# Kernel tuning notes

Hardware: AMD Instinct MI355X
Metric: run time of the kernel (lower is better)

## Reference

```python
import jax, jax.numpy as jnp
import numpy as np

B, S, HID = 1, 2048, 2048
NH, NKV, HD = 32, 8, 64
INTER = 8192
EPS = 1e-6


def rmsnorm(x, w, eps=EPS):
    xf = x.astype(jnp.float32)
    inv = jax.lax.rsqrt(jnp.mean(xf * xf, axis=-1, keepdims=True) + eps)
    return (xf * inv * w).astype(x.dtype)


def rope(x, sin_t, cos_t):
    # x: [B, S, H, D]; sin/cos: [S, D//2]
    sin = sin_t[None, :, None, :]
    cos = cos_t[None, :, None, :]
    d2 = x.shape[-1] // 2
    x0, x1 = x[..., :d2], x[..., d2:]
    return jnp.concatenate((x0 * cos - x1 * sin, x0 * sin + x1 * cos), axis=-1)


def setup_inputs() -> dict:
    key = jax.random.key(0)
    ks = jax.random.split(key, 12)
    hidden_states = jax.random.normal(ks[0], (B, S, HID), dtype=jnp.float32)
    # realistic RoPE tables
    inv_freq = 1.0 / (10000.0 ** (np.arange(0, HD // 2, dtype=np.float32) * 2.0 / HD))
    ang = np.arange(S, dtype=np.float32)[:, None] * inv_freq[None, :]
    sin_table = jnp.asarray(np.sin(ang))
    cos_table = jnp.asarray(np.cos(ang))
    s = 0.02
    return {
        "hidden_states": hidden_states,
        "sin_table": sin_table,
        "cos_table": cos_table,
        "ln1_w": jnp.ones((HID,), jnp.float32),
        "ln2_w": jnp.ones((HID,), jnp.float32),
        "wq": jax.random.normal(ks[1], (HID, NH * HD), jnp.float32) * s,
        "wk": jax.random.normal(ks[2], (HID, NKV * HD), jnp.float32) * s,
        "wv": jax.random.normal(ks[3], (HID, NKV * HD), jnp.float32) * s,
        "wo": jax.random.normal(ks[4], (NH * HD, HID), jnp.float32) * s,
        "w_gate": jax.random.normal(ks[5], (HID, INTER), jnp.float32) * s,
        "w_up": jax.random.normal(ks[6], (HID, INTER), jnp.float32) * s,
        "w_down": jax.random.normal(ks[7], (INTER, HID), jnp.float32) * s,
    }


def attention(x, sin_t, cos_t, wq, wk, wv, wo):
    b, s, _ = x.shape
    q = (x @ wq).reshape(b, s, NH, HD)
    k = (x @ wk).reshape(b, s, NKV, HD)
    v = (x @ wv).reshape(b, s, NKV, HD).transpose(0, 2, 1, 3)  # [B,Hk,S,D]
    q = rope(q, sin_t, cos_t).transpose(0, 2, 1, 3)  # [B,Hq,S,D]
    k = rope(k, sin_t, cos_t).transpose(0, 2, 1, 3)  # [B,Hk,S,D]
    g = NH // NKV
    k = jnp.repeat(k, g, axis=1)
    v = jnp.repeat(v, g, axis=1)
    scale = 1.0 / np.sqrt(HD)
    scores = jnp.einsum("bhqd,bhkd->bhqk", q, k) * scale
    mask = jnp.tril(jnp.ones((s, s), dtype=bool))
    scores = jnp.where(mask, scores, -jnp.inf)
    probs = jax.nn.softmax(scores, axis=-1)
    out = jnp.einsum("bhqk,bhkd->bhqd", probs, v)
    out = out.transpose(0, 2, 1, 3).reshape(b, s, NH * HD)
    return out @ wo


def reference(hidden_states, sin_table, cos_table, ln1_w, ln2_w, wq, wk, wv, wo, w_gate, w_up, w_down):
    x = hidden_states
    x = x + attention(rmsnorm(x, ln1_w), sin_table, cos_table, wq, wk, wv, wo)
    h = rmsnorm(x, ln2_w)
    x = x + (jax.nn.silu(h @ w_gate) * (h @ w_up)) @ w_down
    return x
```

## Files before the change

kernel.cpp:

```cpp
#include <hip/hip_runtime.h>
#include <hip/hip_bf16.h>

typedef float f32x4 __attribute__((ext_vector_type(4)));
typedef unsigned int u32x4 __attribute__((ext_vector_type(4)));
typedef unsigned int u32x2 __attribute__((ext_vector_type(2)));
typedef _Float16 f16x4 __attribute__((ext_vector_type(4)));
typedef unsigned short u16;

#define S_LEN 2048
#define HID 2048
#define NHEAD 32
#define NKVH 8
#define HDIM 64

__device__ __forceinline__ unsigned short f2bf_bits(float f) {
    unsigned int u = __builtin_bit_cast(unsigned int, f);
    unsigned int r = u + 0x7fffu + ((u >> 16) & 1u);
    return (unsigned short)(r >> 16);
}
__device__ __forceinline__ float bf2f(unsigned short b) {
    unsigned int u = ((unsigned int)b) << 16;
    return __builtin_bit_cast(float, u);
}
__device__ __forceinline__ unsigned cvt_pk_bf16(float lo, float hi) {
    unsigned d;
    asm("v_cvt_pk_bf16_f32 %0, %1, %2" : "=v"(d) : "v"(lo), "v"(hi));
    return d;
}

__device__ __forceinline__ f32x4 mfma_bf16(u32x4 a, u32x4 b, f32x4 c) {
    asm("v_mfma_f32_16x16x32_bf16 %0, %1, %2, %0" : "+v"(c) : "v"(a), "v"(b));
    return c;
}

__device__ __forceinline__ void gload_lds16(const void* g, void* l) {
    __builtin_amdgcn_global_load_lds(
        (const __attribute__((address_space(1))) void*)g,
        (__attribute__((address_space(3))) void*)l, 16, 0, 0);
}

__global__ __launch_bounds__(256)
void rmsnorm_k(const float* __restrict__ x, const float* __restrict__ wgt,
               unsigned short* __restrict__ out)
{
    int row = blockIdx.x;
    int t = threadIdx.x;
    const float* xr = x + (size_t)row * HID;
    f32x4 a = *(const f32x4*)(xr + t * 8);
    f32x4 b = *(const f32x4*)(xr + t * 8 + 4);
    float s = 0.f;
#pragma unroll
    for (int i = 0; i < 4; ++i) s += a[i] * a[i] + b[i] * b[i];
#pragma unroll
    for (int off = 32; off > 0; off >>= 1) s += __shfl_down(s, off);
    __shared__ float red[4];
    if ((t & 63) == 0) red[t >> 6] = s;
    __syncthreads();
    float tot = red[0] + red[1] + red[2] + red[3];
    float inv = rsqrtf(tot * (1.0f / (float)HID) + 1e-6f);
    f32x4 wa = *(const f32x4*)(wgt + t * 8);
    f32x4 wb = *(const f32x4*)(wgt + t * 8 + 4);
    unsigned int pk[4];
#pragma unroll
    for (int i = 0; i < 2; ++i) {
        pk[i]     = (unsigned)f2bf_bits(a[2*i] * inv * wa[2*i]) |
                    ((unsigned)f2bf_bits(a[2*i+1] * inv * wa[2*i+1]) << 16);
        pk[i + 2] = (unsigned)f2bf_bits(b[2*i] * inv * wb[2*i]) |
                    ((unsigned)f2bf_bits(b[2*i+1] * inv * wb[2*i+1]) << 16);
    }
    u32x4 ov; ov[0] = pk[0]; ov[1] = pk[1]; ov[2] = pk[2]; ov[3] = pk[3];
    *(u32x4*)(out + (size_t)row * HID + t * 8) = ov;
}

__global__ __launch_bounds__(256)
void transpose_cvt(const float* __restrict__ in, unsigned short* __restrict__ out,
                   int K, int N)
{
    __shared__ unsigned short tile[64 * 65];
    int kb = blockIdx.y * 64, nb = blockIdx.x * 64;
    int t = threadIdx.x;
    int r = t >> 2, c0 = (t & 3) * 16;
    const float* src = in + (size_t)(kb + r) * N + nb + c0;
#pragma unroll
    for (int j = 0; j < 4; ++j) {
        f32x4 v = *(const f32x4*)(src + j * 4);
#pragma unroll
        for (int i = 0; i < 4; ++i)
            tile[r * 65 + c0 + j * 4 + i] = f2bf_bits(v[i]);
    }
    __syncthreads();
    unsigned short e[16];
#pragma unroll
    for (int j = 0; j < 16; ++j) e[j] = tile[(c0 + j) * 65 + r];
    u32x4 o0, o1;
#pragma unroll
    for (int j = 0; j < 4; ++j) {
        o0[j] = (unsigned)e[2*j] | ((unsigned)e[2*j+1] << 16);
        o1[j] = (unsigned)e[8 + 2*j] | ((unsigned)e[8 + 2*j+1] << 16);
    }
    unsigned short* dst = out + (size_t)(nb + r) * K + kb + c0;
    *(u32x4*)(dst) = o0;
    *(u32x4*)(dst + 8) = o1;
}

__global__ __launch_bounds__(256)
void rope_k(unsigned short* __restrict__ qkv, const float* __restrict__ sin_t,
            const float* __restrict__ cos_t)
{
    int s = blockIdx.x;
    for (int it = threadIdx.x; it < (NHEAD + NKVH) * 32; it += 256) {
        int slot = it >> 5;
        int d = it & 31;
        int col = (slot < NHEAD) ? slot * 64 + d : HID + (slot - NHEAD) * 64 + d;
        unsigned short* p = qkv + (size_t)s * 3072 + col;
        float x0 = bf2f(p[0]);
        float x1 = bf2f(p[32]);
        float c = cos_t[s * 32 + d];
        float sn = sin_t[s * 32 + d];
        p[0]  = f2bf_bits(x0 * c - x1 * sn);
        p[32] = f2bf_bits(x0 * sn + x1 * c);
    }
}

__global__ __launch_bounds__(256)
void transpose_v(const unsigned short* __restrict__ qkv, unsigned short* __restrict__ vT)
{
    __shared__ unsigned short tile[64][80];
    int kb = blockIdx.x * 64, kvh = blockIdx.y;
    int t = threadIdx.x;
    int r = t >> 2, c0 = (t & 3) * 16;
    const unsigned short* src = qkv + (size_t)(kb + r) * 3072 + 2560 + kvh * 64 + c0;
    u32x4 v0 = *(const u32x4*)(src);
    u32x4 v1 = *(const u32x4*)(src + 8);
    *(u32x4*)&tile[r][c0] = v0;
    *(u32x4*)&tile[r][c0 + 8] = v1;
    __syncthreads();
    int d = t >> 2, k0 = (t & 3) * 16;
    unsigned short e[16];
#pragma unroll
    for (int j = 0; j < 16; ++j) e[j] = tile[k0 + j][d];
    u32x4 o0, o1;
#pragma unroll
    for (int j = 0; j < 4; ++j) {
        o0[j] = (unsigned)e[2*j] | ((unsigned)e[2*j+1] << 16);
        o1[j] = (unsigned)e[8 + 2*j] | ((unsigned)e[8 + 2*j+1] << 16);
    }
    int s0 = ((k0 >> 3) ^ (d & 7)) & 7;
    int s1 = (((k0 >> 3) + 1) ^ (d & 7)) & 7;
    unsigned short* dst = vT + ((size_t)kvh * 64 + d) * 2048 + kb;
    *(u32x4*)(dst + s0 * 8) = o0;
    *(u32x4*)(dst + s1 * 8) = o1;
}

template <int EPI>
__global__ __launch_bounds__(256)
void gemm_bt(const unsigned short* __restrict__ A,
             const unsigned short* __restrict__ Bt,
             void* __restrict__ outp, const void* __restrict__ auxp,
             int M, int N, int Kc, int lda)
{
    __shared__ unsigned short As[2][128 * 32];
    __shared__ unsigned short Bs[2][128 * 32];
    int t = threadIdx.x, w = t >> 6, l = t & 63;
    int rb = blockIdx.y, cb = blockIdx.x, zb = blockIdx.z;
    int wr = w >> 1, wc = w & 1;
    int l4 = l >> 4, l15 = l & 15;
    int arow = l >> 2, acol = (l & 3) * 8;
    f32x4 acc[4][4] = {};
    const unsigned short* Ag = A + (size_t)rb * 128 * lda + (size_t)zb * Kc
                                 + (size_t)(w * 16 + arow) * lda + acol;
    const unsigned short* Bg = Bt + (size_t)cb * 128 * lda + (size_t)zb * Kc
                                 + (size_t)(w * 16 + arow) * lda + acol;
    int nk = Kc >> 5;

#define STAGE(buf, kt)                                                          \
    {                                                                           \
        const unsigned short* Agk = Ag + (size_t)(kt) * 32;                     \
        const unsigned short* Bgk = Bg + (size_t)(kt) * 32;                     \
        gload_lds16(Agk, &As[buf][w * 512]);                                    \
        gload_lds16(Agk + (size_t)64 * lda, &As[buf][(4 + w) * 512]);           \
        gload_lds16(Bgk, &Bs[buf][w * 512]);                                    \
        gload_lds16(Bgk + (size_t)64 * lda, &Bs[buf][(4 + w) * 512]);           \
    }

    STAGE(0, 0);
    __syncthreads();
    int cur = 0;
    for (int kt = 0; kt < nk; ++kt) {
        if (kt + 1 < nk) STAGE(cur ^ 1, kt + 1);
        u32x4 af[4], bfr[4];
#pragma unroll
        for (int i = 0; i < 4; ++i)
            af[i] = *(const u32x4*)(&As[cur][(wr * 64 + i * 16 + l15) * 32 + l4 * 8]);
#pragma unroll
        for (int n = 0; n < 4; ++n)
            bfr[n] = *(const u32x4*)(&Bs[cur][(wc * 64 + n * 16 + l15) * 32 + l4 * 8]);
#pragma unroll
        for (int i = 0; i < 4; ++i)
#pragma unroll
            for (int n = 0; n < 4; ++n)
                acc[i][n] = mfma_bf16(af[i], bfr[n], acc[i][n]);
        __syncthreads();
        cur ^= 1;
    }
#undef STAGE

    int row0 = rb * 128 + wr * 64 + l4 * 4;
    int col0 = cb * 128 + wc * 64 + l15;
#pragma unroll
    for (int i = 0; i < 4; ++i) {
#pragma unroll
        for (int n = 0; n < 4; ++n) {
#pragma unroll
            for (int r = 0; r < 4; ++r) {
                int row = row0 + i * 16 + r;
                int col = col0 + n * 16;
                size_t idx = (size_t)row * N + col;
                float v = acc[i][n][r];
                if (EPI == 0) {
                    ((unsigned short*)outp)[idx] = f2bf_bits(v);
                } else if (EPI == 3) {
                    ((float*)outp)[idx] = v + ((const float*)auxp)[idx];
                } else {
                    ((_Float16*)outp)[(size_t)zb * M * N + idx] = (_Float16)v;
                }
            }
        }
    }
}

template <int KK, int QUAD, int WAITN>
__device__ __forceinline__ void phase8(u16* lds, int cur, f32x4 (&acc)[8][4],
                                       u32x4 (&bfv)[4],
                                       int aoff, int boff,
                                       const u16* Asrc, const u16* Bsrc,
                                       int lda, int kt_next, bool dostage,
                                       int dst0, int dst1)
{
    const u16* ah = lds + (cur * 4 + KK * 2) * 8192 + aoff + QUAD * 2048;
    u32x4 af[4];
#pragma unroll
    for (int mi = 0; mi < 4; ++mi) af[mi] = *(const u32x4*)(ah + mi * 512);
    if (QUAD == 0) {
        const u16* bh = lds + (cur * 4 + KK * 2 + 1) * 8192 + boff;
#pragma unroll
        for (int ni = 0; ni < 4; ++ni) bfv[ni] = *(const u32x4*)(bh + ni * 512);
    }
    if (dostage) {
        const u16* src = (QUAD ? Bsrc : Asrc) + (size_t)kt_next * 64 + KK * 32;
        u16* d = lds + ((cur ^ 1) * 4 + (KK * 2 + QUAD)) * 8192;
        gload_lds16(src, d + dst0);
        gload_lds16(src + (size_t)128 * lda, d + dst1);
    }
    __builtin_amdgcn_s_barrier();
    asm volatile("s_waitcnt lgkmcnt(0)" ::: "memory");
    __builtin_amdgcn_sched_barrier(0);
    __builtin_amdgcn_s_setprio(1);
#pragma unroll
    for (int mi = 0; mi < 4; ++mi)
#pragma unroll
        for (int ni = 0; ni < 4; ++ni)
            acc[QUAD * 4 + mi][ni] = mfma_bf16(af[mi], bfv[ni], acc[QUAD * 4 + mi][ni]);
    __builtin_amdgcn_s_setprio(0);
    if (WAITN == 4) asm volatile("s_waitcnt vmcnt(4)" ::: "memory");
    else if (WAITN == 0) asm volatile("s_waitcnt vmcnt(0)" ::: "memory");
    __builtin_amdgcn_s_barrier();
}

template <int EPI>
__global__ __launch_bounds__(512, 2)
void gemm8p(const u16* __restrict__ A, const u16* __restrict__ Bt,
            void* __restrict__ outp, const void* __restrict__ auxp,
            int M, int N, int Kc, int lda)
{
    extern __shared__ u16 lds[];
    const int tid = threadIdx.x;
    const int w = tid >> 6, l = tid & 63;
    const int wm = w >> 2, wn = w & 3;
    const int l4 = l >> 4, l15 = l & 15;
    const int zb = blockIdx.y;

    int wg = blockIdx.x, nwg = gridDim.x;
    int swzb = ((nwg & 7) == 0) ? ((wg & 7) * (nwg >> 3) + (wg >> 3)) : wg;
    int rbs = M >> 8;
    int rb = swzb % rbs, cb = swzb / rbs;

    const int sw = ((tid & 3) ^ ((tid >> 3) & 3)) * 8;
    const int srow = tid >> 2;
    const u16* Asrc = A + (size_t)(rb * 256 + srow) * lda + (size_t)zb * Kc + sw;
    const u16* Bsrc = Bt + (size_t)(cb * 256 + srow) * lda + (size_t)zb * Kc + sw;
    const int dst0 = tid * 8, dst1 = (512 + tid) * 8;

    const int rswz = (l15 >> 1) & 3;
    const int aoff = (wm * 128 + l15) * 32 + (l4 ^ rswz) * 8;
    const int boff = (wn * 64 + l15) * 32 + (l4 ^ rswz) * 8;

    f32x4 acc[8][4] = {};
    u32x4 bfv[4];
    const int NT = Kc >> 6;

#pragma unroll
    for (int h = 0; h < 2; ++h) {
        const u16* sA = Asrc + h * 32;
        const u16* sB = Bsrc + h * 32;
        gload_lds16(sA, lds + (h * 2) * 8192 + dst0);
        gload_lds16(sA + (size_t)128 * lda, lds + (h * 2) * 8192 + dst1);
        gload_lds16(sB, lds + (h * 2 + 1) * 8192 + dst0);
        gload_lds16(sB + (size_t)128 * lda, lds + (h * 2 + 1) * 8192 + dst1);
    }
    asm volatile("s_waitcnt vmcnt(4)" ::: "memory");
    __builtin_amdgcn_s_barrier();

    for (int t = 0; t < NT - 1; ++t) {
        int cur = t & 1;
        phase8<0, 0, -1>(lds, cur, acc, bfv, aoff, boff, Asrc, Bsrc, lda, t + 1, true, dst0, dst1);
        phase8<0, 1,  4>(lds, cur, acc, bfv, aoff, boff, Asrc, Bsrc, lda, t + 1, true, dst0, dst1);
        phase8<1, 0, -1>(lds, cur, acc, bfv, aoff, boff, Asrc, Bsrc, lda, t + 1, true, dst0, dst1);
        phase8<1, 1,  4>(lds, cur, acc, bfv, aoff, boff, Asrc, Bsrc, lda, t + 1, true, dst0, dst1);
    }
    {
        int cur = (NT - 1) & 1;
        phase8<0, 0, -1>(lds, cur, acc, bfv, aoff, boff, Asrc, Bsrc, lda, 0, false, dst0, dst1);
        phase8<0, 1,  0>(lds, cur, acc, bfv, aoff, boff, Asrc, Bsrc, lda, 0, false, dst0, dst1);
        phase8<1, 0, -1>(lds, cur, acc, bfv, aoff, boff, Asrc, Bsrc, lda, 0, false, dst0, dst1);
        phase8<1, 1, -1>(lds, cur, acc, bfv, aoff, boff, Asrc, Bsrc, lda, 0, false, dst0, dst1);
    }

    int row0 = rb * 256 + wm * 128 + l4 * 4;
    int col0 = cb * 256 + wn * 64 + l15;
#pragma unroll
    for (int mi = 0; mi < 8; ++mi) {
#pragma unroll
        for (int ni = 0; ni < 4; ++ni) {
#pragma unroll
            for (int r = 0; r < 4; ++r) {
                int row = row0 + mi * 16 + r;
                int col = col0 + ni * 16;
                size_t idx = (size_t)row * N + col;
                float v = acc[mi][ni][r];
                if (EPI == 1) {
                    float sv = v / (1.0f + __expf(-v));
                    ((unsigned short*)outp)[idx] = f2bf_bits(sv);
                } else if (EPI == 2) {
                    float gv = bf2f(((const unsigned short*)auxp)[idx]);
                    ((unsigned short*)outp)[idx] = f2bf_bits(v * gv);
                } else {
                    ((_Float16*)outp)[(size_t)zb * M * N + idx] = (_Float16)v;
                }
            }
        }
    }
}

__global__ __launch_bounds__(256)
void reduce_add4(float* __restrict__ out, const _Float16* __restrict__ p, int n)
{
    int i = (blockIdx.x * 256 + threadIdx.x) * 4;
    f32x4 a = *(const f32x4*)(out + i);
#pragma unroll
    for (int z = 0; z < 4; ++z) {
        f16x4 h = *(const f16x4*)(p + (size_t)z * n + i);
#pragma unroll
        for (int j = 0; j < 4; ++j) a[j] += (float)h[j];
    }
    *(f32x4*)(out + i) = a;
}

__global__ __launch_bounds__(256)
void reduce_res2(float* __restrict__ out, const float* __restrict__ x,
                 const _Float16* __restrict__ p, int n)
{
    int i = (blockIdx.x * 256 + threadIdx.x) * 4;
    f32x4 a = *(const f32x4*)(x + i);
#pragma unroll
    for (int z = 0; z < 2; ++z) {
        f16x4 h = *(const f16x4*)(p + (size_t)z * n + i);
#pragma unroll
        for (int j = 0; j < 4; ++j) a[j] += (float)h[j];
    }
    *(f32x4*)(out + i) = a;
}

__global__ __launch_bounds__(256)
void attn_fwd(const unsigned short* __restrict__ qkv,
              const unsigned short* __restrict__ vT,
              unsigned short* __restrict__ out)
{
    int p = blockIdx.x, h = blockIdx.y, kvh = h >> 2;
    int t = threadIdx.x, w = t >> 6, l = t & 63;
    int l4 = l >> 4, l15 = l & 15;
    __shared__ unsigned short Ks[2][64 * 64];
    __shared__ unsigned short Vs[2][64 * 64];

    const unsigned short* Kg = qkv + HID + kvh * 64;
    const unsigned short* Vg = vT + (size_t)kvh * 64 * 2048;

    int ch0 = w * 2, ch1 = w * 2 + 1;
    int rsub = l >> 3;
    int ksw = ((l & 7) ^ (rsub & 7)) * 8;
    int vcol = (l & 7) * 8;
    int sw0 = (l4 ^ (l15 & 7)) * 8;
    int sw1 = ((l4 | 4) ^ (l15 & 7)) * 8;
    int srcA = ((l >> 4) & 1) * 32 + l15;
    int srcB = srcA + 16;
    bool hi32 = (l & 32) != 0;

#define STAGE_KV(buf, kt)                                                         \
    {                                                                             \
        gload_lds16(Kg + (size_t)((kt) * 64 + ch0 * 8 + rsub) * 3072 + ksw,       \
                    &Ks[buf][ch0 * 512]);                                         \
        gload_lds16(Kg + (size_t)((kt) * 64 + ch1 * 8 + rsub) * 3072 + ksw,       \
                    &Ks[buf][ch1 * 512]);                                         \
        gload_lds16(Vg + (size_t)(ch0 * 8 + rsub) * 2048 + (kt) * 64 + vcol,      \
                    &Vs[buf][ch0 * 512]);                                         \
        gload_lds16(Vg + (size_t)(ch1 * 8 + rsub) * 2048 + (kt) * 64 + vcol,      \
                    &Vs[buf][ch1 * 512]);                                         \
    }

    const float SC2 = 0.18033688f;
    const float THR = 44.36f;
    const float BIG = -3.0e38f;

    for (int half = 0; half < 2; ++half) {
        int qb = half ? (31 - p) : p;
        int qrow0 = qb * 64 + w * 16;
        STAGE_KV(0, 0);
        const unsigned short* qg = qkv + (size_t)(qrow0 + l15) * 3072 + h * 64 + l4 * 8;
        u32x4 aq0 = *(const u32x4*)(qg);
        u32x4 aq1 = *(const u32x4*)(qg + 32);
        f32x4 o[4] = {};
        float m = BIG, ls = 0.f;
        __syncthreads();
        int cur = 0;
        for (int kt = 0; kt <= qb; ++kt) {
            if (kt < qb) STAGE_KV(cur ^ 1, kt + 1);
            f32x4 sc[4];
#pragma unroll
            for (int n = 0; n < 4; ++n) {
                const unsigned short* kb_ = &Ks[cur][(n * 16 + l15) * 64];
                u32x4 b0 = *(const u32x4*)(kb_ + sw0);
                u32x4 b1 = *(const u32x4*)(kb_ + sw1);
                f32x4 z = {};
                z = mfma_bf16(b0, aq0, z);
                z = mfma_bf16(b1, aq1, z);
                sc[n] = z;
            }
            if (kt == qb) {
                int qloc = w * 16 + l15;
#pragma unroll
                for (int n = 0; n < 4; ++n)
#pragma unroll
                    for (int r = 0; r < 4; ++r)
                        if (n * 16 + l4 * 4 + r > qloc) sc[n][r] = BIG;
            }
            float rmax = BIG;
#pragma unroll
            for (int n = 0; n < 4; ++n)
#pragma unroll
                for (int r = 0; r < 4; ++r) rmax = fmaxf(rmax, sc[n][r]);
            rmax = fmaxf(rmax, __shfl_xor(rmax, 16));
            rmax = fmaxf(rmax, __shfl_xor(rmax, 32));
            if (__ballot(rmax - m > THR)) {
                float mn = fmaxf(m, rmax);
                float al = __builtin_exp2f((m - mn) * SC2);
                m = mn;
                ls *= al;
#pragma unroll
                for (int nd = 0; nd < 4; ++nd)
#pragma unroll
                    for (int r = 0; r < 4; ++r) o[nd][r] *= al;
            }
            float ms = m * SC2, rs = 0.f;
#pragma unroll
            for (int n = 0; n < 4; ++n)
#pragma unroll
                for (int r = 0; r < 4; ++r) {
                    float pe = __builtin_exp2f(__builtin_fmaf(sc[n][r], SC2, -ms));
                    sc[n][r] = pe;
                    rs += pe;
                }
            rs += __shfl_xor(rs, 16);
            rs += __shfl_xor(rs, 32);
            ls += rs;
            unsigned pk0[2], pk1[2], pk2[2], pk3[2];
#pragma unroll
            for (int rr = 0; rr < 2; ++rr) {
                pk0[rr] = cvt_pk_bf16(sc[0][2*rr], sc[0][2*rr+1]);
                pk1[rr] = cvt_pk_bf16(sc[1][2*rr], sc[1][2*rr+1]);
                pk2[rr] = cvt_pk_bf16(sc[2][2*rr], sc[2][2*rr+1]);
                pk3[rr] = cvt_pk_bf16(sc[3][2*rr], sc[3][2*rr+1]);
            }
            u32x4 W1, W2;
            {
                unsigned a0, a1;
                a0 = __shfl(pk0[0], srcA); a1 = __shfl(pk1[0], srcA); W1[0] = hi32 ? a1 : a0;
                a0 = __shfl(pk0[1], srcA); a1 = __shfl(pk1[1], srcA); W1[1] = hi32 ? a1 : a0;
                a0 = __shfl(pk0[0], srcB); a1 = __shfl(pk1[0], srcB); W1[2] = hi32 ? a1 : a0;
                a0 = __shfl(pk0[1], srcB); a1 = __shfl(pk1[1], srcB); W1[3] = hi32 ? a1 : a0;
                a0 = __shfl(pk2[0], srcA); a1 = __shfl(pk3[0], srcA); W2[0] = hi32 ? a1 : a0;
                a0 = __shfl(pk2[1], srcA); a1 = __shfl(pk3[1], srcA); W2[1] = hi32 ? a1 : a0;
                a0 = __shfl(pk2[0], srcB); a1 = __shfl(pk3[0], srcB); W2[2] = hi32 ? a1 : a0;
                a0 = __shfl(pk2[1], srcB); a1 = __shfl(pk3[1], srcB); W2[3] = hi32 ? a1 : a0;
            }
#pragma unroll
            for (int nd = 0; nd < 4; ++nd) {
                const unsigned short* vb = &Vs[cur][(nd * 16 + l15) * 64];
                u32x4 bv0 = *(const u32x4*)(vb + sw0);
                u32x4 bv1 = *(const u32x4*)(vb + sw1);
                o[nd] = mfma_bf16(bv0, W1, o[nd]);
                o[nd] = mfma_bf16(bv1, W2, o[nd]);
            }
            __syncthreads();
            cur ^= 1;
        }
#undef STAGE_KV
        float linv = 1.0f / ls;
        unsigned short* orow = out + (size_t)(qrow0 + l15) * HID + h * 64 + l4 * 4;
#pragma unroll
        for (int nd = 0; nd < 4; ++nd) {
            u32x2 wv;
            wv[0] = cvt_pk_bf16(o[nd][0] * linv, o[nd][1] * linv);
            wv[1] = cvt_pk_bf16(o[nd][2] * linv, o[nd][3] * linv);
            *(u32x2*)(orow + nd * 16) = wv;
        }
    }
}

extern "C" void kernel_launch(void* const* d_in, const int* in_sizes, int n_in,
                              void* d_out, int out_size, void* d_ws, size_t ws_size,
                              hipStream_t stream)
{
    const float* x     = (const float*)d_in[0];
    const float* sin_t = (const float*)d_in[1];
    const float* cos_t = (const float*)d_in[2];
    const float* ln1w  = (const float*)d_in[3];
    const float* ln2w  = (const float*)d_in[4];
    const float* wq    = (const float*)d_in[5];
    const float* wk    = (const float*)d_in[6];
    const float* wv    = (const float*)d_in[7];
    const float* wo    = (const float*)d_in[8];
    const float* wg    = (const float*)d_in[9];
    const float* wu    = (const float*)d_in[10];
    const float* wd    = (const float*)d_in[11];
    float* out = (float*)d_out;

    char* ws = (char*)d_ws;
    if (ws_size < 113246208u) return;
    unsigned short* wT   = (unsigned short*)(ws);
    unsigned short* xn   = (unsigned short*)(ws + 33554432u);
    unsigned short* qkv  = (unsigned short*)(ws + 41943040u);
    unsigned short* attn = (unsigned short*)(ws + 54525952u);
    unsigned short* vT   = (unsigned short*)(ws + 62914560u);
    _Float16*       part = (_Float16*)(ws + 33554432u);
    unsigned short* g    = (unsigned short*)(ws + 79691776u);
    _Float16*       opart = (_Float16*)(ws + 79691776u);

    hipFuncSetAttribute(reinterpret_cast<const void*>(&gemm8p<1>),
                        hipFuncAttributeMaxDynamicSharedMemorySize, 131072);
    hipFuncSetAttribute(reinterpret_cast<const void*>(&gemm8p<2>),
                        hipFuncAttributeMaxDynamicSharedMemorySize, 131072);
    hipFuncSetAttribute(reinterpret_cast<const void*>(&gemm8p<5>),
                        hipFuncAttributeMaxDynamicSharedMemorySize, 131072);

    rmsnorm_k<<<S_LEN, 256, 0, stream>>>(x, ln1w, xn);

    transpose_cvt<<<dim3(32, 32), 256, 0, stream>>>(wq, wT, 2048, 2048);
    transpose_cvt<<<dim3(8, 32), 256, 0, stream>>>(wk, wT + (size_t)2048 * 2048, 2048, 512);
    transpose_cvt<<<dim3(8, 32), 256, 0, stream>>>(wv, wT + (size_t)2560 * 2048, 2048, 512);

    gemm_bt<0><<<dim3(24, 16, 1), 256, 0, stream>>>(xn, wT, qkv, nullptr, 2048, 3072, 2048, 2048);

    rope_k<<<S_LEN, 256, 0, stream>>>(qkv, sin_t, cos_t);
    transpose_v<<<dim3(32, 8), 256, 0, stream>>>(qkv, vT);

    attn_fwd<<<dim3(16, 32), 256, 0, stream>>>(qkv, vT, attn);

    transpose_cvt<<<dim3(32, 32), 256, 0, stream>>>(wo, wT, 2048, 2048);
    gemm_bt<5><<<dim3(16, 16, 2), 256, 0, stream>>>(attn, wT, opart, nullptr, 2048, 2048, 1024, 2048);
    reduce_res2<<<4096, 256, 0, stream>>>(out, x, opart, 4194304);

    rmsnorm_k<<<S_LEN, 256, 0, stream>>>(out, ln2w, xn);

    transpose_cvt<<<dim3(128, 32), 256, 0, stream>>>(wg, wT, 2048, 8192);
    gemm8p<1><<<dim3(256, 1), 512, 131072, stream>>>(xn, wT, g, nullptr, 2048, 8192, 2048, 2048);

    transpose_cvt<<<dim3(128, 32), 256, 0, stream>>>(wu, wT, 2048, 8192);
    gemm8p<2><<<dim3(256, 1), 512, 131072, stream>>>(xn, wT, g, g, 2048, 8192, 2048, 2048);

    transpose_cvt<<<dim3(32, 128), 256, 0, stream>>>(wd, wT, 8192, 2048);
    gemm8p<5><<<dim3(64, 4), 512, 131072, stream>>>(g, wT, part, nullptr, 2048, 2048, 2048, 8192);

    reduce_add4<<<4096, 256, 0, stream>>>(out, part, 4194304);
}
```

Before: 450.4 us.

## Deepen gemm8p global-to-LDS prefetch pipeline to stage half-tiles further ahead

Restructures the 256x256 GEMM main loop so each half-k slice is prefetched roughly one and a half tiles ahead instead of one tile, reusing the current buffer's freed first-half slot for tile t+2. The prologue now issues three half-tile loads and waits with vmcnt(8), giving more outstanding global loads to hide memory latency. The tail special case is removed: every iteration stages, and out-of-range stages reload tile 0 as dummy traffic. This adds wasted loads at the end and relies on the freed-slot reuse being correctly ordered by the barriers.

```diff
diff --git a/kernel.cpp b/kernel.cpp
--- a/kernel.cpp
+++ b/kernel.cpp
@@ -229,12 +229,12 @@
     }
 }
 
-template <int KK, int QUAD, int WAITN>
+template <int KK, int QUAD>
 __device__ __forceinline__ void phase8(u16* lds, int cur, f32x4 (&acc)[8][4],
                                        u32x4 (&bfv)[4],
                                        int aoff, int boff,
                                        const u16* Asrc, const u16* Bsrc,
-                                       int lda, int kt_next, bool dostage,
+                                       int lda, int kt_stage,
                                        int dst0, int dst1)
 {
     const u16* ah = lds + (cur * 4 + KK * 2) * 8192 + aoff + QUAD * 2048;
@@ -246,9 +246,11 @@
 #pragma unroll
         for (int ni = 0; ni < 4; ++ni) bfv[ni] = *(const u32x4*)(bh + ni * 512);
     }
-    if (dostage) {
-        const u16* src = (QUAD ? Bsrc : Asrc) + (size_t)kt_next * 64 + KK * 32;
-        u16* d = lds + ((cur ^ 1) * 4 + (KK * 2 + QUAD)) * 8192;
+    {
+        const u16* src = (QUAD ? Bsrc : Asrc) + (size_t)kt_stage * 64 + (KK == 0 ? 32 : 0);
+        int dbuf = (KK == 0) ? (cur ^ 1) : cur;
+        int slot = (KK == 0) ? (2 + QUAD) : QUAD;
+        u16* d = lds + (dbuf * 4 + slot) * 8192;
         gload_lds16(src, d + dst0);
         gload_lds16(src + (size_t)128 * lda, d + dst1);
     }
@@ -262,8 +264,7 @@
         for (int ni = 0; ni < 4; ++ni)
             acc[QUAD * 4 + mi][ni] = mfma_bf16(af[mi], bfv[ni], acc[QUAD * 4 + mi][ni]);
     __builtin_amdgcn_s_setprio(0);
-    if (WAITN == 4) asm volatile("s_waitcnt vmcnt(4)" ::: "memory");
-    else if (WAITN == 0) asm volatile("s_waitcnt vmcnt(0)" ::: "memory");
+    if (QUAD == 1) asm volatile("s_waitcnt vmcnt(8)" ::: "memory");
     __builtin_amdgcn_s_barrier();
 }
 
@@ -299,32 +300,37 @@
     u32x4 bfv[4];
     const int NT = Kc >> 6;
 
-#pragma unroll
-    for (int h = 0; h < 2; ++h) {
-        const u16* sA = Asrc + h * 32;
-        const u16* sB = Bsrc + h * 32;
-        gload_lds16(sA, lds + (h * 2) * 8192 + dst0);
-        gload_lds16(sA + (size_t)128 * lda, lds + (h * 2) * 8192 + dst1);
-        gload_lds16(sB, lds + (h * 2 + 1) * 8192 + dst0);
-        gload_lds16(sB + (size_t)128 * lda, lds + (h * 2 + 1) * 8192 + dst1);
-    }
-    asm volatile("s_waitcnt vmcnt(4)" ::: "memory");
+    {
+#pragma unroll
+        for (int h = 0; h < 2; ++h) {
+            const u16* sA = Asrc + h * 32;
+            const u16* sB = Bsrc + h * 32;
+            gload_lds16(sA, lds + (h * 2) * 8192 + dst0);
+            gload_lds16(sA + (size_t)128 * lda, lds + (h * 2) * 8192 + dst1);
+            gload_lds16(sB, lds + (h * 2 + 1) * 8192 + dst0);
+            gload_lds16(sB + (size_t)128 * lda, lds + (h * 2 + 1) * 8192 + dst1);
+        }
+        int t1 = (NT > 1) ? 1 : 0;
+        const u16* sA = Asrc + (size_t)t1 * 64;
+        const u16* sB = Bsrc + (size_t)t1 * 64;
+        gload_lds16(sA, lds + (4 + 0) * 8192 + dst0);
+        gload_lds16(sA + (size_t)128 * lda, lds + (4 + 0) * 8192 + dst1);
+        gload_lds16(sB, lds + (4 + 1) * 8192 + dst0);
+        gload_lds16(sB + (size_t)128 * lda, lds + (4 + 1) * 8192 + dst1);
+    }
+    asm volatile("s_waitcnt vmcnt(8)" ::: "memory");
     __builtin_amdgcn_s_barrier();
 
-    for (int t = 0; t < NT - 1; ++t) {
+    for (int t = 0; t < NT; ++t) {
         int cur = t & 1;
-        phase8<0, 0, -1>(lds, cur, acc, bfv, aoff, boff, Asrc, Bsrc, lda, t + 1, true, dst0, dst1);
-        phase8<0, 1,  4>(lds, cur, acc, bfv, aoff, boff, Asrc, Bsrc, lda, t + 1, true, dst0, dst1);
-        phase8<1, 0, -1>(lds, cur, acc, bfv, aoff, boff, Asrc, Bsrc, lda, t + 1, true, dst0, dst1);
-        phase8<1, 1,  4>(lds, cur, acc, bfv, aoff, boff, Asrc, Bsrc, lda, t + 1, true, dst0, dst1);
-    }
-    {
-        int cur = (NT - 1) & 1;
-        phase8<0, 0, -1>(lds, cur, acc, bfv, aoff, boff, Asrc, Bsrc, lda, 0, false, dst0, dst1);
-        phase8<0, 1,  0>(lds, cur, acc, bfv, aoff, boff, Asrc, Bsrc, lda, 0, false, dst0, dst1);
-        phase8<1, 0, -1>(lds, cur, acc, bfv, aoff, boff, Asrc, Bsrc, lda, 0, false, dst0, dst1);
-        phase8<1, 1, -1>(lds, cur, acc, bfv, aoff, boff, Asrc, Bsrc, lda, 0, false, dst0, dst1);
-    }
+        int k1 = (t + 1 < NT) ? t + 1 : 0;
+        int k2 = (t + 2 < NT) ? t + 2 : 0;
+        phase8<0, 0>(lds, cur, acc, bfv, aoff, boff, Asrc, Bsrc, lda, k1, dst0, dst1);
+        phase8<0, 1>(lds, cur, acc, bfv, aoff, boff, Asrc, Bsrc, lda, k1, dst0, dst1);
+        phase8<1, 0>(lds, cur, acc, bfv, aoff, boff, Asrc, Bsrc, lda, k2, dst0, dst1);
+        phase8<1, 1>(lds, cur, acc, bfv, aoff, boff, Asrc, Bsrc, lda, k2, dst0, dst1);
+    }
+    asm volatile("s_waitcnt vmcnt(0)" ::: "memory");
 
     int row0 = rb * 256 + wm * 128 + l4 * 4;
     int col0 = cb * 256 + wn * 64 + l15;
```

Result: no change. 450.0 us (-0.1%).
